# Optimization experiments

Hardware: AMD Instinct MI355X
Metric: run time of the kernel (lower is better)

Reference implementation:

```python
import jax, jax.numpy as jnp
import numpy as np

C = 512
CQ = C // 8
BN_EPS = 1e-5


def setup_inputs() -> dict:
    key = jax.random.key(0)
    ks = jax.random.split(key, 12)
    s = 0.02
    return {
        "x": jax.random.normal(ks[0], (4, C, 64, 64), dtype=jnp.float32),
        "qw": jax.random.normal(ks[1], (CQ, C), dtype=jnp.float32) * s,
        "qb": jnp.zeros((CQ,), dtype=jnp.float32),
        "kw": jax.random.normal(ks[2], (CQ, C), dtype=jnp.float32) * s,
        "kb": jnp.zeros((CQ,), dtype=jnp.float32),
        "vw": jax.random.normal(ks[3], (C, C), dtype=jnp.float32) * s,
        "vb": jnp.zeros((C,), dtype=jnp.float32),
        "gamma": jnp.zeros((1,), dtype=jnp.float32),
        "beta": jnp.zeros((1,), dtype=jnp.float32),
        "fw": jax.random.normal(ks[4], (C, 2 * C), dtype=jnp.float32) * s,
        "fb": jnp.zeros((C,), dtype=jnp.float32),
        "bn_w": jnp.ones((C,), dtype=jnp.float32),
        "bn_b": jnp.zeros((C,), dtype=jnp.float32),
    }


def reference(x, qw, qb, kw, kb, vw, vb, gamma, beta, fw, fb, bn_w, bn_b):
    b, c, h, w = x.shape
    n = h * w
    xf = x.reshape(b, c, n)  # [b, c, n]

    # ----- position attention -----
    q = jnp.einsum('oc,bcn->bon', qw, xf) + qb[None, :, None]  # [b, cq, n]
    k = jnp.einsum('oc,bcn->bon', kw, xf) + kb[None, :, None]
    v = jnp.einsum('oc,bcn->bon', vw, xf) + vb[None, :, None]  # [b, c, n]
    # scores[i, j] = q_i . k_j, softmax over j
    scores = jnp.einsum('bci,bcj->bij', q, k)  # [b, n, n]
    att = jax.nn.softmax(scores, axis=-1)
    pos = jnp.einsum('bcj,bij->bci', v, att)  # [b, c, n]
    pos_out = (gamma[0] * pos + xf).reshape(b, c, h, w)

    # ----- channel attention -----
    energy = jnp.einsum('bin,bjn->bij', xf, xf)  # [b, c, c]
    catt = jax.nn.softmax(energy, axis=-1)
    chan = jnp.einsum('bij,bjn->bin', catt, xf)
    chan_out = (beta[0] * chan + xf).reshape(b, c, h, w)

    # ----- fusion: 1x1 conv + BN (batch stats, training mode) + ReLU -----
    cat = jnp.concatenate([pos_out, chan_out], axis=1)  # [b, 2c, h, w]
    y = jnp.einsum('oc,bchw->bohw', fw, cat) + fb[None, :, None, None]
    mean = jnp.mean(y, axis=(0, 2, 3), keepdims=True)
    var = jnp.var(y, axis=(0, 2, 3), keepdims=True)
    yn = (y - mean) * jax.lax.rsqrt(var + BN_EPS)
    out = jax.nn.relu(yn * bn_w[None, :, None, None] + bn_b[None, :, None, None])
    return out
```

## Files before the change

### kernel.cpp

```cpp
#include <hip/hip_runtime.h>
#include <stdint.h>

typedef unsigned short u16;
typedef __attribute__((ext_vector_type(8))) short bf16x8;
typedef __attribute__((ext_vector_type(4))) float f32x4;

#define DEVI static __device__ __forceinline__

DEVI u16 f2bf(float f){
  union { float f; uint32_t u; } c; c.f = f;
  uint32_t u = c.u;
  u += 0x7FFFu + ((u >> 16) & 1u);
  return (u16)(u >> 16);
}
DEVI float b2f(u16 h){
  union { uint32_t u; float f; } c; c.u = ((uint32_t)h) << 16;
  return c.f;
}

DEVI void gload16(const u16* g, u16* l){
  __builtin_amdgcn_global_load_lds(
      (const __attribute__((address_space(1))) unsigned int*)g,
      (__attribute__((address_space(3))) unsigned int*)l, 16, 0, 0);
}

DEVI bf16x8 ldsrd(const void* base, int byte){
  return *reinterpret_cast<const bf16x8*>((const char*)base + byte);
}

template<int BM,int BN,int FM,int FN,int BIAS,int EPI,int SWZ,int KSPLIT=1>
__global__ __launch_bounds__(256) void gemm_bt(
    const u16* __restrict__ A, long long strideA, int lda,
    const u16* __restrict__ B, long long strideB, int ldb,
    void* __restrict__ C, long long strideC, int ldc,
    const float* __restrict__ bias, int K,
    const float* __restrict__ cscale, const u16* __restrict__ xadd,
    long long strideX, int ldx)
{
  constexpr int BK  = 32;
  constexpr int WTM = FM*16, WTN = FN*16;
  static_assert(BM == 2*WTM && BN == 2*WTN, "2x2 wave layout");
  __shared__ u16 As[BM*BK];
  __shared__ u16 Bs[BN*BK];

  int bx = blockIdx.x, by = blockIdx.y, bz = blockIdx.z;
  if(SWZ){
    const int gx = gridDim.x, gy = gridDim.y;
    const int nwg = gx * gy * gridDim.z;
    const int orig = bx + gx * (by + gy * bz);
    const int q = nwg >> 3, r = nwg & 7;
    const int xcd = orig & 7, i = orig >> 3;
    const int wg = (xcd < r ? xcd*(q+1) : r*(q+1) + (xcd-r)*q) + i;
    bx = wg % gx;
    const int t = wg / gx;
    by = t % gy;
    bz = t / gy;
  }

  const int zz = bz;
  const int z  = (KSPLIT > 1) ? zz / KSPLIT : zz;
  const int ks = (KSPLIT > 1) ? zz % KSPLIT : 0;
  const u16* Ab = A + (long long)z * strideA + (long long)ks * K;
  const u16* Bb = B + (long long)z * strideB + (long long)ks * K;

  const int tid  = threadIdx.x;
  const int lane = tid & 63, wid = tid >> 6;
  const int wr = wid >> 1, wc = wid & 1;
  const long long bm0 = (long long)by * BM;
  const long long bn0 = (long long)bx * BN;

  const int srow  = lane >> 2;
  const int scol  = (((lane & 3) ^ ((lane >> 3) & 3))) * 8;
  const int wrow  = wid * 16 + srow;
  constexpr int TA = BM/64, TB = BN/64;

  const int fr  = lane & 15;
  const int sl8 = ((lane >> 4) ^ ((lane >> 1) & 3)) * 8;

  f32x4 acc[FM][FN] = {};

  for(int k0 = 0; k0 < K; k0 += BK){
    __syncthreads();
    #pragma unroll
    for(int t=0;t<TA;t++)
      gload16(&Ab[(bm0 + t*64 + wrow)*lda + k0 + scol],
              &As[(t*64 + wid*16)*BK]);
    #pragma unroll
    for(int t=0;t<TB;t++)
      gload16(&Bb[(bn0 + t*64 + wrow)*ldb + k0 + scol],
              &Bs[(t*64 + wid*16)*BK]);
    __syncthreads();

    bf16x8 af[FM], bg[FN];
    #pragma unroll
    for(int m=0;m<FM;m++)
      af[m] = *reinterpret_cast<const bf16x8*>(&As[(wr*WTM + m*16 + fr)*BK + sl8]);
    #pragma unroll
    for(int n=0;n<FN;n++)
      bg[n] = *reinterpret_cast<const bf16x8*>(&Bs[(wc*WTN + n*16 + fr)*BK + sl8]);
    #pragma unroll
    for(int m=0;m<FM;m++)
      #pragma unroll
      for(int n=0;n<FN;n++)
        acc[m][n] = __builtin_amdgcn_mfma_f32_16x16x32_bf16(af[m], bg[n], acc[m][n], 0, 0, 0);
  }

  const int lr = (lane >> 4) * 4, lc = lane & 15;
  const float g = (EPI == 3) ? cscale[0] : 0.f;
  #pragma unroll
  for(int m=0;m<FM;m++){
    #pragma unroll
    for(int n=0;n<FN;n++){
      #pragma unroll
      for(int r=0;r<4;r++){
        long long row = bm0 + wr*WTM + m*16 + lr + r;
        long long col = bn0 + wc*WTN + n*16 + lc;
        float v = acc[m][n][r];
        if(BIAS == 1) v += bias[(int)row];
        if(BIAS == 2) v += bias[(int)col];
        long long idx = row * (long long)ldc + col;
        if(EPI == 0){
          ((float*)C + (long long)zz*strideC)[idx] = v;
        } else if(EPI == 1){
          ((float*)C + (long long)zz*strideC)[idx] += v;
        } else if(EPI == 2){
          ((u16*)C + (long long)zz*strideC)[idx] = f2bf(v);
        } else {
          float xv = b2f(xadd[(long long)z*strideX + row*(long long)ldx + col]);
          ((u16*)C + (long long)zz*strideC)[idx] = f2bf(g * v + xv);
        }
      }
    }
  }
}

__global__ __launch_bounds__(512, 4) void flash_pos(
    const u16* __restrict__ qkT,
    const u16* __restrict__ vB,
    const u16* __restrict__ xfT,
    u16* __restrict__ pcT,
    const float* __restrict__ gamma)
{
  __shared__ u16 Ks[2][64*64];
  __shared__ u16 Vs[256*64];
  __shared__ u16 Ps[64*64];
  __shared__ float RS[2][4][32];

  int flat = blockIdx.x + 64*(blockIdx.y + 2*blockIdx.z);
  flat = (flat & 7)*64 + (flat >> 3);
  const int bx = flat & 63;
  const int ch = (flat >> 6) & 1;
  const int z  = flat >> 7;

  const int q0 = bx*64, c0 = ch*256;
  const int tid = threadIdx.x, lane = tid & 63, wid = tid >> 6;
  const int wr = wid >> 2, wc = wid & 3;
  const int fr = lane & 15, fq = lane >> 4;

  const u16* qkb = qkT + (long long)z*4096*128;
  const u16* vbb = vB  + (long long)z*512*4096;

  const int srow  = lane >> 3;
  const int sslot = (lane & 7) ^ srow;

  bf16x8 qa[2][2];
  #pragma unroll
  for(int m=0;m<2;m++)
    #pragma unroll
    for(int kk=0;kk<2;kk++)
      qa[m][kk] = *reinterpret_cast<const bf16x8*>(
          &qkb[(long long)(q0 + wr*32 + m*16 + fr)*128 + kk*32 + fq*8]);

  const u16* kp  = qkb + (long long)(wid*8 + srow)*128 + 64 + sslot*8;
  const u16* vp0 = vbb + (long long)(c0 + wid*8 + srow)*4096 + sslot*8;

  const int xm   = (fr & 7) << 4;
  const int koff = (wc*16 + fr)*128 + ((fq*16) ^ xm);
  const int pab  = (wr*32 + fr)*128 + ((fq*16) ^ xm);
  const int vfb  = (wc*64 + fr)*128 + ((fq*16) ^ xm);
  const int kdst = wid * 1024;
  const int key2 = (wc*16 + fr)*2;
  int pwo[4];
  #pragma unroll
  for(int r=0;r<4;r++){
    int qr = fq*4 + r;
    pwo[r] = qr*128 + (key2 ^ ((qr & 7) << 4));
  }

  gload16(kp, (u16*)((char*)Ks + kdst));
  kp += 64*128;
  gload16(vp0,            &Vs[(  0 + wid*8)*64]);
  gload16(vp0 +  64*4096, &Vs[( 64 + wid*8)*64]);
  gload16(vp0 + 128*4096, &Vs[(128 + wid*8)*64]);
  gload16(vp0 + 192*4096, &Vs[(192 + wid*8)*64]);
  vp0 += 64;
  __syncthreads();

  f32x4 acc[2][4] = {};
  float rsacc[2][4] = {};

  for(int t=0;t<64;t++){
    const int kbase = (t & 1) ? 8192 : 0;
    bf16x8 kb0 = ldsrd(Ks, kbase + koff);
    bf16x8 kb1 = ldsrd(Ks, kbase + (koff ^ 64));
    f32x4 s[2] = {};
    #pragma unroll
    for(int m=0;m<2;m++){
      s[m] = __builtin_amdgcn_mfma_f32_16x16x32_bf16(qa[m][0], kb0, s[m], 0, 0, 0);
      s[m] = __builtin_amdgcn_mfma_f32_16x16x32_bf16(qa[m][1], kb1, s[m], 0, 0, 0);
    }

    #pragma unroll
    for(int m=0;m<2;m++){
      #pragma unroll
      for(int r=0;r<4;r++){
        float e = __expf(s[m][r]);
        rsacc[m][r] += e;
        *(u16*)((char*)Ps + (pwo[r] + wr*4096 + m*2048)) = f2bf(e);
      }
    }
    __syncthreads();

    if(t+1 < 64){
      gload16(kp, (u16*)((char*)Ks + (kbase ^ 8192) + kdst));
      kp += 64*128;
    }

    bf16x8 pa00 = ldsrd(Ps, pab);
    bf16x8 pa01 = ldsrd(Ps, pab ^ 64);
    bf16x8 pa10 = ldsrd(Ps, (pab + 2048));
    bf16x8 pa11 = ldsrd(Ps, (pab + 2048) ^ 64);
    __builtin_amdgcn_s_setprio(1);
    #pragma unroll
    for(int n=0;n<4;n++){
      bf16x8 v0 = ldsrd(Vs, vfb + n*2048);
      bf16x8 v1 = ldsrd(Vs, (vfb + n*2048) ^ 64);
      acc[0][n] = __builtin_amdgcn_mfma_f32_16x16x32_bf16(pa00, v0, acc[0][n], 0, 0, 0);
      acc[0][n] = __builtin_amdgcn_mfma_f32_16x16x32_bf16(pa01, v1, acc[0][n], 0, 0, 0);
      acc[1][n] = __builtin_amdgcn_mfma_f32_16x16x32_bf16(pa10, v0, acc[1][n], 0, 0, 0);
      acc[1][n] = __builtin_amdgcn_mfma_f32_16x16x32_bf16(pa11, v1, acc[1][n], 0, 0, 0);
    }
    __builtin_amdgcn_s_setprio(0);
    __syncthreads();

    if(t+1 < 64){
      gload16(vp0,            &Vs[(  0 + wid*8)*64]);
      gload16(vp0 +  64*4096, &Vs[( 64 + wid*8)*64]);
      gload16(vp0 + 128*4096, &Vs[(128 + wid*8)*64]);
      gload16(vp0 + 192*4096, &Vs[(192 + wid*8)*64]);
      vp0 += 64;
    }
  }

  #pragma unroll
  for(int m=0;m<2;m++)
    #pragma unroll
    for(int r=0;r<4;r++){
      float v = rsacc[m][r];
      #pragma unroll
      for(int o=1;o<16;o<<=1) v += __shfl_xor(v, o);
      rsacc[m][r] = v;
    }
  if(fr == 0){
    #pragma unroll
    for(int m=0;m<2;m++)
      #pragma unroll
      for(int r=0;r<4;r++)
        RS[wr][wc][m*16 + fq*4 + r] = rsacc[m][r];
  }
  __syncthreads();

  const float g = gamma[0];
  #pragma unroll
  for(int m=0;m<2;m++){
    float inv[4];
    #pragma unroll
    for(int r=0;r<4;r++){
      int rloc = m*16 + fq*4 + r;
      inv[r] = g / (RS[wr][0][rloc] + RS[wr][1][rloc] +
                    RS[wr][2][rloc] + RS[wr][3][rloc]);
    }
    #pragma unroll
    for(int n=0;n<4;n++){
      #pragma unroll
      for(int r=0;r<4;r++){
        int qrow = q0 + wr*32 + m*16 + fq*4 + r;
        int c    = c0 + wc*64 + n*16 + fr;
        float xv = b2f(xfT[((long long)z*4096 + qrow)*512 + c]);
        pcT[((long long)z*4096 + qrow)*1024 + c] = f2bf(acc[m][n][r]*inv[r] + xv);
      }
    }
  }
}

__global__ __launch_bounds__(256) void softmax_sum8b(const u16* __restrict__ part,
                                                     u16* __restrict__ catt)
{
  const int row = blockIdx.x;
  const int b = row >> 9, i = row & 511;
  const int t = threadIdx.x;
  const int lane = t & 63, wid = t >> 6;
  float v0 = 0.f, v1 = 0.f;
  #pragma unroll
  for(int sl=0;sl<8;sl++){
    uint32_t pr = *reinterpret_cast<const uint32_t*>(
        &part[(((long long)(b*8 + sl)*512 + i)*512) + 2*t]);
    v0 += b2f((u16)pr);
    v1 += b2f((u16)(pr >> 16));
  }
  float m = fmaxf(v0, v1);
  #pragma unroll
  for(int o=32;o;o>>=1) m = fmaxf(m, __shfl_xor(m, o));
  __shared__ float sred[4];
  if(lane == 0) sred[wid] = m;
  __syncthreads();
  m = fmaxf(fmaxf(sred[0], sred[1]), fmaxf(sred[2], sred[3]));
  float e0 = __expf(v0 - m), e1 = __expf(v1 - m);
  float s = e0 + e1;
  #pragma unroll
  for(int o=32;o;o>>=1) s += __shfl_xor(s, o);
  __syncthreads();
  if(lane == 0) sred[wid] = s;
  __syncthreads();
  s = sred[0] + sred[1] + sred[2] + sred[3];
  float inv = 1.0f / s;
  uint32_t pk = (uint32_t)f2bf(e0 * inv) | ((uint32_t)f2bf(e1 * inv) << 16);
  *reinterpret_cast<uint32_t*>(&catt[(long long)row * 512 + 2*t]) = pk;
}

__global__ __launch_bounds__(256) void prep_weights(
    const float* __restrict__ qw, const float* __restrict__ kw,
    const float* __restrict__ vw, const float* __restrict__ fw,
    const float* __restrict__ qb, const float* __restrict__ kb,
    u16* __restrict__ qkwb, u16* __restrict__ vwb, u16* __restrict__ fwb,
    float* __restrict__ qkb)
{
  long long i = (long long)blockIdx.x*256 + threadIdx.x;
  const float* src; u16* dst; long long o;
  if(i < 8192){        src = qw; dst = qkwb;          o = i; }
  else if(i < 16384){  src = kw; dst = qkwb + 32768;  o = i - 8192; }
  else if(i < 81920){  src = vw; dst = vwb;           o = i - 16384; }
  else if(i < 212992){ src = fw; dst = fwb;           o = i - 81920; }
  else if(i < 213024){
    int t = (int)(i - 212992) * 4;
    #pragma unroll
    for(int j=0;j<4;j++) qkb[t+j] = (t+j < 64) ? qb[t+j] : kb[t+j-64];
    return;
  } else return;
  float4 v = reinterpret_cast<const float4*>(src)[o];
  ushort4 w;
  w.x = f2bf(v.x); w.y = f2bf(v.y); w.z = f2bf(v.z); w.w = f2bf(v.w);
  reinterpret_cast<ushort4*>(dst)[o] = w;
}

__global__ __launch_bounds__(256) void transpose_cast(
    const float* __restrict__ x, u16* __restrict__ xfb, u16* __restrict__ xfT)
{
  __shared__ float tile[32][33];
  const int b  = blockIdx.z;
  const int n0 = blockIdx.x * 32, c0 = blockIdx.y * 32;
  const int tx = threadIdx.x, ty = threadIdx.y;
  const float* xp = x + (long long)b * 512 * 4096;
  #pragma unroll
  for(int i=0;i<4;i++){
    int c = c0 + ty + i*8;
    float v = xp[(long long)c*4096 + n0 + tx];
    tile[ty + i*8][tx] = v;
    xfb[((long long)b*512 + c)*4096 + n0 + tx] = f2bf(v);
  }
  __syncthreads();
  #pragma unroll
  for(int i=0;i<4;i++){
    int n = n0 + ty + i*8;
    xfT[((long long)b*4096 + n)*512 + c0 + tx] = f2bf(tile[tx][ty + i*8]);
  }
}

__global__ __launch_bounds__(256) void bn_stats(const float* __restrict__ y,
                                                float* __restrict__ stat)
{
  const int o = blockIdx.x, t = threadIdx.x;
  const int lane = t & 63, wid = t >> 6;
  float s = 0.f, ss = 0.f;
  for(int b=0;b<4;b++){
    const float* p = y + ((long long)b*512 + o)*4096;
    for(int i=t;i<4096;i+=256){ float v = p[i]; s += v; ss += v*v; }
  }
  #pragma unroll
  for(int off=32;off;off>>=1){ s += __shfl_xor(s, off); ss += __shfl_xor(ss, off); }
  __shared__ float sred[8];
  if(lane == 0){ sred[wid] = s; sred[wid+4] = ss; }
  __syncthreads();
  if(t == 0){
    float S  = sred[0]+sred[1]+sred[2]+sred[3];
    float SS = sred[4]+sred[5]+sred[6]+sred[7];
    float mean = S * (1.f/16384.f);
    float var  = SS * (1.f/16384.f) - mean*mean;
    stat[o*2]   = mean;
    stat[o*2+1] = rsqrtf(var + 1e-5f);
  }
}

__global__ __launch_bounds__(256) void bn_apply(float* __restrict__ y,
    const float* __restrict__ stat, const float* __restrict__ w,
    const float* __restrict__ bb)
{
  long long i = (long long)blockIdx.x*256 + threadIdx.x;
  float4 v = reinterpret_cast<float4*>(y)[i];
  int o = (int)(((i*4) >> 12) & 511);
  float mean = stat[o*2], rstd = stat[o*2+1];
  float sc = w[o] * rstd;
  float sh = bb[o] - mean * sc;
  v.x = fmaxf(v.x*sc + sh, 0.f);
  v.y = fmaxf(v.y*sc + sh, 0.f);
  v.z = fmaxf(v.z*sc + sh, 0.f);
  v.w = fmaxf(v.w*sc + sh, 0.f);
  reinterpret_cast<float4*>(y)[i] = v;
}

extern "C" void kernel_launch(void* const* d_in, const int* in_sizes, int n_in,
                              void* d_out, int out_size, void* d_ws, size_t ws_size,
                              hipStream_t stream)
{
  const float* x     = (const float*)d_in[0];
  const float* qw    = (const float*)d_in[1];
  const float* qb    = (const float*)d_in[2];
  const float* kw    = (const float*)d_in[3];
  const float* kb    = (const float*)d_in[4];
  const float* vw    = (const float*)d_in[5];
  const float* vb    = (const float*)d_in[6];
  const float* gamma = (const float*)d_in[7];
  const float* beta  = (const float*)d_in[8];
  const float* fw    = (const float*)d_in[9];
  const float* fb    = (const float*)d_in[10];
  const float* bnw   = (const float*)d_in[11];
  const float* bnb   = (const float*)d_in[12];
  float* out = (float*)d_out;
  (void)in_sizes; (void)n_in; (void)out_size; (void)ws_size;

  char* base = (char*)d_ws;
  size_t off = 0;
  auto alloc = [&](size_t bytes)->char* {
    char* p = base + off;
    off += (bytes + 255) & ~(size_t)255;
    return p;
  };
  const long long NB = 4, Cc = 512, Nn = 4096;

  u16*   xfT  = (u16*)alloc((size_t)NB*Nn*Cc*2);
  u16*   xfb  = (u16*)alloc((size_t)NB*Cc*Nn*2);
  u16*   qkwb = (u16*)alloc((size_t)128*Cc*2);
  float* qkb  = (float*)alloc(128*4);
  u16*   vwb  = (u16*)alloc((size_t)Cc*Cc*2);
  u16*   fwb  = (u16*)alloc((size_t)Cc*2*Cc*2);
  u16*   qkT  = (u16*)alloc((size_t)NB*Nn*128*2);
  u16*   vB   = (u16*)alloc((size_t)NB*Cc*Nn*2);
  u16*   pcT  = (u16*)alloc((size_t)NB*Nn*1024*2);
  u16*   epart= (u16*)alloc((size_t)32*Cc*Cc*2);
  u16*   catt = (u16*)alloc((size_t)NB*Cc*Cc*2);
  float* stat = (float*)alloc((size_t)Cc*2*4);

  prep_weights<<<dim3(833), dim3(256), 0, stream>>>(qw, kw, vw, fw, qb, kb,
                                                    qkwb, vwb, fwb, qkb);
  transpose_cast<<<dim3(128,16,4), dim3(32,8), 0, stream>>>(x, xfb, xfT);

  gemm_bt<64,128,2,4,2,2,1><<<dim3(1,64,4), dim3(256), 0, stream>>>(
      xfT, Nn*Cc, 512, qkwb, 0, 512, qkT, Nn*128, 128, qkb, 512,
      nullptr, nullptr, 0, 0);
  gemm_bt<128,128,4,4,1,2,1><<<dim3(32,4,4), dim3(256), 0, stream>>>(
      vwb, 0, 512, xfT, Nn*Cc, 512, vB, Cc*Nn, 4096, vb, 512,
      nullptr, nullptr, 0, 0);

  gemm_bt<128,128,4,4,0,2,1,8><<<dim3(4,4,32), dim3(256), 0, stream>>>(
      xfb, Cc*Nn, 4096, xfb, Cc*Nn, 4096, epart, Cc*Cc, 512, nullptr, 512,
      nullptr, nullptr, 0, 0);
  softmax_sum8b<<<dim3(2048), dim3(256), 0, stream>>>(epart, catt);
  gemm_bt<128,128,4,4,0,3,1><<<dim3(4,32,4), dim3(256), 0, stream>>>(
      xfT, Nn*Cc, 512, catt, Cc*Cc, 512, pcT + 512, Nn*1024, 1024, nullptr, 512,
      beta, xfT, Nn*Cc, 512);

  flash_pos<<<dim3(64,2,4), dim3(512), 0, stream>>>(qkT, vB, xfT, pcT, gamma);

  gemm_bt<128,128,4,4,1,0,1><<<dim3(32,4,4), dim3(256), 0, stream>>>(
      fwb, 0, 1024, pcT, Nn*1024, 1024, out, Cc*Nn, 4096, fb, 1024,
      nullptr, nullptr, 0, 0);

  bn_stats<<<dim3(512), dim3(256), 0, stream>>>(out, stat);
  bn_apply<<<dim3(8192), dim3(256), 0, stream>>>(out, stat, bnw, bnb);
}
```

Baseline: 251.4 us.

## Fuse BN partial statistics into fusion GEMM epilogue and store output as bf16

The final 1x1-conv GEMM now writes its result as bf16 into a reused workspace region. Its epilogue also reduces per-row sum and sum-of-squares partials into a small buffer. This replaces the full-tensor bn_stats pass with a tiny finalize kernel. The apply kernel reads bf16 and writes fp32 to the output, which removes one fp32 read pass and halves the intermediate write, at the cost of rounding pre-BN activations to bf16. The finalize kernel reads partials with a per-thread serial strided loop, which may be latency-bound.

```diff
diff --git a/kernel.cpp b/kernel.cpp
--- a/kernel.cpp
+++ b/kernel.cpp
@@ -35,7 +35,7 @@
     void* __restrict__ C, long long strideC, int ldc,
     const float* __restrict__ bias, int K,
     const float* __restrict__ cscale, const u16* __restrict__ xadd,
-    long long strideX, int ldx)
+    long long strideX, int ldx, float* __restrict__ red)
 {
   constexpr int BK  = 32;
   constexpr int WTM = FM*16, WTN = FN*16;
@@ -106,6 +106,35 @@
   }
 
   const int lr = (lane >> 4) * 4, lc = lane & 15;
+
+  if(EPI == 7){
+    u16* Cp = (u16*)C + (long long)zz*strideC;
+    #pragma unroll
+    for(int m=0;m<FM;m++){
+      #pragma unroll
+      for(int r=0;r<4;r++){
+        long long row = bm0 + wr*WTM + m*16 + lr + r;
+        float bv = bias[(int)row];
+        float s = 0.f, ss = 0.f;
+        #pragma unroll
+        for(int n=0;n<FN;n++){
+          long long col = bn0 + wc*WTN + n*16 + lc;
+          float v = acc[m][n][r] + bv;
+          Cp[row*(long long)ldc + col] = f2bf(v);
+          s += v; ss += v*v;
+        }
+        #pragma unroll
+        for(int o=1;o<16;o<<=1){ s += __shfl_xor(s, o); ss += __shfl_xor(ss, o); }
+        if(lc == 0){
+          int slot = (z*(int)gridDim.x + bx)*2 + wc;
+          red[(int)row*512 + slot*2]     = s;
+          red[(int)row*512 + slot*2 + 1] = ss;
+        }
+      }
+    }
+    return;
+  }
+
   const float g = (EPI == 3) ? cscale[0] : 0.f;
   #pragma unroll
   for(int m=0;m<FM;m++){
@@ -376,46 +405,42 @@
   }
 }
 
-__global__ __launch_bounds__(256) void bn_stats(const float* __restrict__ y,
-                                                float* __restrict__ stat)
-{
-  const int o = blockIdx.x, t = threadIdx.x;
-  const int lane = t & 63, wid = t >> 6;
+__global__ __launch_bounds__(256) void bn_finalize(const float* __restrict__ red,
+                                                   float* __restrict__ stat)
+{
+  int ch = blockIdx.x*256 + threadIdx.x;
+  if(ch >= 512) return;
   float s = 0.f, ss = 0.f;
-  for(int b=0;b<4;b++){
-    const float* p = y + ((long long)b*512 + o)*4096;
-    for(int i=t;i<4096;i+=256){ float v = p[i]; s += v; ss += v*v; }
-  }
-  #pragma unroll
-  for(int off=32;off;off>>=1){ s += __shfl_xor(s, off); ss += __shfl_xor(ss, off); }
-  __shared__ float sred[8];
-  if(lane == 0){ sred[wid] = s; sred[wid+4] = ss; }
-  __syncthreads();
-  if(t == 0){
-    float S  = sred[0]+sred[1]+sred[2]+sred[3];
-    float SS = sred[4]+sred[5]+sred[6]+sred[7];
-    float mean = S * (1.f/16384.f);
-    float var  = SS * (1.f/16384.f) - mean*mean;
-    stat[o*2]   = mean;
-    stat[o*2+1] = rsqrtf(var + 1e-5f);
-  }
-}
-
-__global__ __launch_bounds__(256) void bn_apply(float* __restrict__ y,
+  for(int j=0;j<256;j++){
+    s  += red[ch*512 + j*2];
+    ss += red[ch*512 + j*2 + 1];
+  }
+  float mean = s * (1.f/16384.f);
+  float var  = ss * (1.f/16384.f) - mean*mean;
+  stat[ch*2]   = mean;
+  stat[ch*2+1] = rsqrtf(var + 1e-5f);
+}
+
+__global__ __launch_bounds__(256) void bn_apply_b(const u16* __restrict__ y,
     const float* __restrict__ stat, const float* __restrict__ w,
-    const float* __restrict__ bb)
+    const float* __restrict__ bb, float* __restrict__ out)
 {
   long long i = (long long)blockIdx.x*256 + threadIdx.x;
-  float4 v = reinterpret_cast<float4*>(y)[i];
-  int o = (int)(((i*4) >> 12) & 511);
-  float mean = stat[o*2], rstd = stat[o*2+1];
-  float sc = w[o] * rstd;
-  float sh = bb[o] - mean * sc;
-  v.x = fmaxf(v.x*sc + sh, 0.f);
-  v.y = fmaxf(v.y*sc + sh, 0.f);
-  v.z = fmaxf(v.z*sc + sh, 0.f);
-  v.w = fmaxf(v.w*sc + sh, 0.f);
-  reinterpret_cast<float4*>(y)[i] = v;
+  bf16x8 v = *reinterpret_cast<const bf16x8*>(&y[i*8]);
+  int o = (int)(((i*8) >> 12) & 511);
+  float sc = w[o] * stat[o*2+1];
+  float sh = bb[o] - stat[o*2] * sc;
+  float4 lo, hi;
+  lo.x = fmaxf(b2f((u16)v[0])*sc + sh, 0.f);
+  lo.y = fmaxf(b2f((u16)v[1])*sc + sh, 0.f);
+  lo.z = fmaxf(b2f((u16)v[2])*sc + sh, 0.f);
+  lo.w = fmaxf(b2f((u16)v[3])*sc + sh, 0.f);
+  hi.x = fmaxf(b2f((u16)v[4])*sc + sh, 0.f);
+  hi.y = fmaxf(b2f((u16)v[5])*sc + sh, 0.f);
+  hi.z = fmaxf(b2f((u16)v[6])*sc + sh, 0.f);
+  hi.w = fmaxf(b2f((u16)v[7])*sc + sh, 0.f);
+  *reinterpret_cast<float4*>(&out[i*8])     = lo;
+  *reinterpret_cast<float4*>(&out[i*8 + 4]) = hi;
 }
 
 extern "C" void kernel_launch(void* const* d_in, const int* in_sizes, int n_in,
@@ -448,17 +473,20 @@
   const long long NB = 4, Cc = 512, Nn = 4096;
 
   u16*   xfT  = (u16*)alloc((size_t)NB*Nn*Cc*2);
+  u16*   fwb  = (u16*)alloc((size_t)Cc*2*Cc*2);
+  char*  region = (char*)(base + off);
   u16*   xfb  = (u16*)alloc((size_t)NB*Cc*Nn*2);
   u16*   qkwb = (u16*)alloc((size_t)128*Cc*2);
   float* qkb  = (float*)alloc(128*4);
   u16*   vwb  = (u16*)alloc((size_t)Cc*Cc*2);
-  u16*   fwb  = (u16*)alloc((size_t)Cc*2*Cc*2);
   u16*   qkT  = (u16*)alloc((size_t)NB*Nn*128*2);
   u16*   vB   = (u16*)alloc((size_t)NB*Cc*Nn*2);
   u16*   pcT  = (u16*)alloc((size_t)NB*Nn*1024*2);
   u16*   epart= (u16*)alloc((size_t)32*Cc*Cc*2);
   u16*   catt = (u16*)alloc((size_t)NB*Cc*Cc*2);
   float* stat = (float*)alloc((size_t)Cc*2*4);
+  float* red  = (float*)alloc((size_t)Cc*256*2*4);
+  u16*   ybf16= (u16*)region;
 
   prep_weights<<<dim3(833), dim3(256), 0, stream>>>(qw, kw, vw, fw, qb, kb,
                                                     qkwb, vwb, fwb, qkb);
@@ -466,25 +494,25 @@
 
   gemm_bt<64,128,2,4,2,2,1><<<dim3(1,64,4), dim3(256), 0, stream>>>(
       xfT, Nn*Cc, 512, qkwb, 0, 512, qkT, Nn*128, 128, qkb, 512,
-      nullptr, nullptr, 0, 0);
+      nullptr, nullptr, 0, 0, nullptr);
   gemm_bt<128,128,4,4,1,2,1><<<dim3(32,4,4), dim3(256), 0, stream>>>(
       vwb, 0, 512, xfT, Nn*Cc, 512, vB, Cc*Nn, 4096, vb, 512,
-      nullptr, nullptr, 0, 0);
+      nullptr, nullptr, 0, 0, nullptr);
 
   gemm_bt<128,128,4,4,0,2,1,8><<<dim3(4,4,32), dim3(256), 0, stream>>>(
       xfb, Cc*Nn, 4096, xfb, Cc*Nn, 4096, epart, Cc*Cc, 512, nullptr, 512,
-      nullptr, nullptr, 0, 0);
+      nullptr, nullptr, 0, 0, nullptr);
   softmax_sum8b<<<dim3(2048), dim3(256), 0, stream>>>(epart, catt);
   gemm_bt<128,128,4,4,0,3,1><<<dim3(4,32,4), dim3(256), 0, stream>>>(
       xfT, Nn*Cc, 512, catt, Cc*Cc, 512, pcT + 512, Nn*1024, 1024, nullptr, 512,
-      beta, xfT, Nn*Cc, 512);
+      beta, xfT, Nn*Cc, 512, nullptr);
 
   flash_pos<<<dim3(64,2,4), dim3(512), 0, stream>>>(qkT, vB, xfT, pcT, gamma);
 
-  gemm_bt<128,128,4,4,1,0,1><<<dim3(32,4,4), dim3(256), 0, stream>>>(
-      fwb, 0, 1024, pcT, Nn*1024, 1024, out, Cc*Nn, 4096, fb, 1024,
-      nullptr, nullptr, 0, 0);
-
-  bn_stats<<<dim3(512), dim3(256), 0, stream>>>(out, stat);
-  bn_apply<<<dim3(8192), dim3(256), 0, stream>>>(out, stat, bnw, bnb);
-}
+  gemm_bt<128,128,4,4,1,7,1><<<dim3(32,4,4), dim3(256), 0, stream>>>(
+      fwb, 0, 1024, pcT, Nn*1024, 1024, ybf16, Cc*Nn, 4096, fb, 1024,
+      nullptr, nullptr, 0, 0, red);
+
+  bn_finalize<<<dim3(2), dim3(256), 0, stream>>>(red, stat);
+  bn_apply_b<<<dim3(4096), dim3(256), 0, stream>>>(ybf16, stat, bnw, bnb, out);
+}
```

Result: no change. 252.7 us (+0.5%).
